# Kernel tuning notes

Measured on AMD Instinct MI355X. Metric: run time of the kernel, lower is better.

The kernel has to match this reference:

```python
import jax, jax.numpy as jnp
import numpy as np

N_P = 2048   # personality nodes
N_W = 89     # word nodes (fixed by user_word_adj[:, :89])
N_ALL = N_P + N_W
B = 16384    # users
E2 = 768     # sentence embedding size
UW = 313     # 89 word cols + 224 extra cols -> 32 + 224 = 256 for share1


def setup_inputs() -> dict:
    key = jax.random.key(0)
    ks = jax.random.split(key, 20)
    rn = lambda k, s, sc=0.1: (jax.random.normal(k, s, jnp.float32) * sc)
    pern_adj = jax.random.randint(ks[2], (N_P, N_P), 0, 2, jnp.int32)
    pern_adj = pern_adj.at[jnp.arange(N_P), jnp.arange(N_P)].set(1)
    word_pern_adj = jax.random.randint(ks[3], (N_ALL, N_ALL), 0, 2, jnp.int32)
    word_pern_adj = word_pern_adj.at[jnp.arange(N_ALL), jnp.arange(N_ALL)].set(1)
    return dict(
        pern_feature=rn(ks[0], (N_P, 256), 1.0),
        word_feature=rn(ks[1], (N_W, 256), 1.0),
        pern_adj=pern_adj,
        word_pern_adj=word_pern_adj,
        user_word_adj=jax.random.uniform(ks[4], (B, UW), jnp.float32),
        sentence_embed=rn(ks[5], (B, E2), 1.0),
        w1=rn(ks[6], (8, 256, 32)), a_src1=rn(ks[7], (8, 32)), a_dst1=rn(ks[8], (8, 32)), bias1=jnp.zeros((32,), jnp.float32),
        w2=rn(ks[9], (8, 256, 32)), a_src2=rn(ks[10], (8, 32)), a_dst2=rn(ks[11], (8, 32)), bias2=jnp.zeros((32,), jnp.float32),
        W_s1=rn(ks[12], (256, 128)), b_s1=jnp.zeros((128,), jnp.float32),
        W_s2=rn(ks[13], (E2, 128)), b_s2=jnp.zeros((128,), jnp.float32),
        W_f1=rn(ks[14], (128, 64)), b_f1=jnp.zeros((64,), jnp.float32),
        W_fa=rn(ks[15], (256, 128)), b_fa=jnp.zeros((128,), jnp.float32),
        W_fb=rn(ks[16], (128, 5)), b_fb=jnp.zeros((5,), jnp.float32),
    )


def gat(h, adj, w, a_src, a_dst, bias):
    # h: (n, f_in); w: (H, f_in, f_out); a_src/a_dst: (H, f_out); adj: (n, n) 0/1
    hp = jnp.einsum('nf,hfo->hno', h, w)                      # (H, n, f_out)
    e_src = jnp.einsum('hno,ho->hn', hp, a_src)               # (H, n)
    e_dst = jnp.einsum('hno,ho->hn', hp, a_dst)               # (H, n)
    e = jax.nn.leaky_relu(e_src[:, :, None] + e_dst[:, None, :], 0.2)  # (H, n, n)
    e = jnp.where(adj[None, :, :] > 0, e, jnp.float32(-1e9))
    attn = jax.nn.softmax(e, axis=-1)
    out = jnp.einsum('hnm,hmo->hno', attn, hp) + bias         # (H, n, f_out)
    return out, attn


def reference(pern_feature, word_feature, pern_adj, word_pern_adj,
              user_word_adj, sentence_embed,
              w1, a_src1, a_dst1, bias1, w2, a_src2, a_dst2, bias2,
              W_s1, b_s1, W_s2, b_s2, W_f1, b_f1, W_fa, b_fa, W_fb, b_fb):
    n_p = pern_feature.shape[0]
    # GAT 1 on personality graph
    h1, attn_pp = gat(pern_feature, pern_adj, w1, a_src1, a_dst1, bias1)
    h1 = jax.nn.elu(jnp.transpose(h1, (1, 0, 2)).reshape(n_p, -1))   # (n_p, 256)
    # dropout is identity at eval time
    h1_wp = jnp.concatenate([word_feature, h1], axis=0)               # (n_w+n_p, 256)
    # GAT 2 on word-personality graph, mean over heads
    h2, attn_wp = gat(h1_wp, word_pern_adj, w2, a_src2, a_dst2, bias2)
    h2 = h2.mean(axis=0)                                              # (n_w+n_p, 32)
    h2_word = h2[:word_feature.shape[0], :]                           # (89, 32)
    # user aggregation over word adjacency + row normalization
    x = user_word_adj[:, :N_W] @ h2_word                              # (B, 32)
    x_c = jnp.concatenate([x, user_word_adj[:, N_W:]], axis=1)        # (B, 256)
    x = x_c / x_c.sum(axis=1, keepdims=True)
    # dual heads
    output1 = x @ W_s1 + b_s1
    output2 = sentence_embed @ W_s2 + b_s2
    output1_new = output1 @ W_f1 + b_f1
    output2_new = output2 @ W_f1 + b_f1
    x_temp = jnp.concatenate([output1, output2], axis=1)
    x_temp = jax.nn.relu(x_temp @ W_fa + b_fa) @ W_fb + b_fb
    return (output1_new, output2_new, x_temp, attn_pp, attn_wp, x)
```

## Files before the change

kernel.cpp:

```cpp
#include <hip/hip_runtime.h>
#include <cstdint>
#include <cstddef>

#define N_P 2048
#define N_W 89
#define N_ALLC 2137
#define BQ 16384
#define E2C 768

typedef __attribute__((ext_vector_type(8))) short short8;
typedef __attribute__((ext_vector_type(4))) float float4v;

__device__ __forceinline__ float waveMax(float v){
#pragma unroll
  for (int o = 32; o > 0; o >>= 1) v = fmaxf(v, __shfl_down(v, o, 64));
  return v;
}
__device__ __forceinline__ float waveSum(float v){
#pragma unroll
  for (int o = 32; o > 0; o >>= 1) v += __shfl_down(v, o, 64);
  return v;
}
__device__ __forceinline__ unsigned short f2bf(float f){
  union { float f; unsigned int u; } v; v.f = f;
  unsigned int u = v.u;
  unsigned int r = (u + 0x7FFFu + ((u >> 16) & 1u)) >> 16;
  return (unsigned short)r;
}
__device__ __forceinline__ short8 cvt8(const float* p){
  float4 f0 = *(const float4*)p;
  float4 f1 = *(const float4*)(p + 4);
  short8 a;
  a[0] = (short)f2bf(f0.x); a[1] = (short)f2bf(f0.y);
  a[2] = (short)f2bf(f0.z); a[3] = (short)f2bf(f0.w);
  a[4] = (short)f2bf(f1.x); a[5] = (short)f2bf(f1.y);
  a[6] = (short)f2bf(f1.z); a[7] = (short)f2bf(f1.w);
  return a;
}

__device__ __forceinline__ void wpk_one(const float* __restrict__ W,
                                        unsigned short* __restrict__ out,
                                        int K, int N, int idx){
  if (idx >= K * N) return;
  int k = idx / N, n = idx - k * N;
  out[((size_t)((k >> 5) * 4 + ((k >> 3) & 3)) * N + n) * 8 + (k & 7)] = f2bf(W[idx]);
}

__global__ __launch_bounds__(256) void repack_all(
    const float* __restrict__ w1, float* __restrict__ wrm1,
    const float* __restrict__ w2, float* __restrict__ wrm2,
    const float* __restrict__ Ws1, unsigned short* __restrict__ ws1pk,
    const float* __restrict__ Ws2, unsigned short* __restrict__ ws2pk,
    const float* __restrict__ Wf1, unsigned short* __restrict__ wf1pk,
    const float* __restrict__ Wfa, unsigned short* __restrict__ wfapk,
    const float* __restrict__ wf, float* __restrict__ h1wp,
    const int* __restrict__ adj1, unsigned long long* __restrict__ bm1,
    const int* __restrict__ adj2, unsigned long long* __restrict__ bm2)
{
  int b = blockIdx.x, t = threadIdx.x;
  if (b < 256) {
    int idx = b * 256 + t;
    int f = idx >> 8, c = idx & 255;
    int h = c >> 5, o = c & 31;
    wrm1[idx] = w1[h * 8192 + f * 32 + o];
  } else if (b < 512) {
    int idx = (b - 256) * 256 + t;
    int f = idx >> 8, c = idx & 255;
    int h = c >> 5, o = c & 31;
    wrm2[idx] = w2[h * 8192 + f * 32 + o];
  } else if (b < 640) {
    wpk_one(Ws1, ws1pk, 256, 128, (b - 512) * 256 + t);
  } else if (b < 1024) {
    wpk_one(Ws2, ws2pk, 768, 128, (b - 640) * 256 + t);
  } else if (b < 1056) {
    wpk_one(Wf1, wf1pk, 128, 64, (b - 1024) * 256 + t);
  } else if (b < 1184) {
    wpk_one(Wfa, wfapk, 256, 128, (b - 1056) * 256 + t);
  } else if (b < 1273) {
    int idx = (b - 1184) * 256 + t;
    if (idx < N_W * 256) h1wp[idx] = wf[idx];
  } else if (b < 1529) {
    int r0 = (b - 1273) * 8;
    int wv = t >> 6, ln = t & 63;
    for (int rr = 0; rr < 8; ++rr) {
      int r = r0 + rr;
      const int* arow = adj1 + (size_t)r * N_P;
      for (int m0 = wv * 64; m0 < N_P; m0 += 256) {
        unsigned long long mask = __ballot(arow[m0 + ln] > 0);
        if (ln == 0) bm1[(size_t)r * 32 + (m0 >> 6)] = mask;
      }
    }
  } else {
    int r0 = (b - 1529) * 8;
    int wv = t >> 6, ln = t & 63;
    for (int rr = 0; rr < 8; ++rr) {
      int r = r0 + rr;
      if (r >= N_ALLC) break;
      const int* arow = adj2 + (size_t)r * N_ALLC;
      for (int m0 = wv * 64; m0 < 2176; m0 += 256) {
        int m = m0 + ln;
        unsigned long long mask = __ballot((m < N_ALLC) && (arow[m] > 0));
        if (ln == 0) bm2[(size_t)r * 34 + (m0 >> 6)] = mask;
      }
    }
  }
}

__global__ __launch_bounds__(256) void gemm_f32(
    const float* __restrict__ A, int lda,
    const float* __restrict__ B, int ldb,
    float* __restrict__ C, int ldc,
    int M, int N, int K)
{
  __shared__ __align__(16) float As[16][68];
  __shared__ __align__(16) float Bs[16][68];
  int t = threadIdx.x;
  int m0 = blockIdx.x * 64, n0 = blockIdx.y * 64;
  int tm = t >> 4, tn = t & 15;
  int ar = t >> 2, ak = (t & 3) * 4;
  int bk = t >> 4, bn = (t & 15) * 4;
  float acc[4][4] = {};
  for (int k0 = 0; k0 < K; k0 += 16) {
    float4 av = {0.f, 0.f, 0.f, 0.f};
    int arow = m0 + ar;
    if (arow < M) av = *(const float4*)(A + (size_t)arow * lda + k0 + ak);
    As[ak][ar] = av.x; As[ak + 1][ar] = av.y; As[ak + 2][ar] = av.z; As[ak + 3][ar] = av.w;
    *(float4*)&Bs[bk][bn] = *(const float4*)(B + (size_t)(k0 + bk) * ldb + n0 + bn);
    __syncthreads();
#pragma unroll
    for (int kk = 0; kk < 16; ++kk) {
      float4 a4 = *(const float4*)&As[kk][tm * 4];
      float4 b4 = *(const float4*)&Bs[kk][tn * 4];
      float a[4] = {a4.x, a4.y, a4.z, a4.w};
      float b[4] = {b4.x, b4.y, b4.z, b4.w};
#pragma unroll
      for (int i = 0; i < 4; ++i)
#pragma unroll
        for (int j = 0; j < 4; ++j) acc[i][j] += a[i] * b[j];
    }
    __syncthreads();
  }
#pragma unroll
  for (int i = 0; i < 4; ++i) {
    int row = m0 + tm * 4 + i;
    if (row < M) {
      float4 v;
      v.x = acc[i][0]; v.y = acc[i][1]; v.z = acc[i][2]; v.w = acc[i][3];
      *(float4*)(C + (size_t)row * ldc + n0 + tn * 4) = v;
    }
  }
}

__global__ __launch_bounds__(256) void esrc_edst(
    const float* __restrict__ hp,
    const float* __restrict__ a_src,
    const float* __restrict__ a_dst,
    float* __restrict__ es, float* __restrict__ ed,
    unsigned short* __restrict__ hppk,
    float* __restrict__ h2w, const float* __restrict__ b2,
    int N, int do_pack)
{
  __shared__ float sa[256], sd[256];
  int t = threadIdx.x;
  sa[t] = a_src[t]; sd[t] = a_dst[t];
  __syncthreads();
  int idx = blockIdx.x * 256 + t;
  if (h2w != nullptr && idx < N_W * 32) h2w[idx] = b2[idx & 31];
  if (idx >= N * 8) return;
  int n = idx >> 3, h = idx & 7;
  const float* hpp = hp + (size_t)n * 256 + h * 32;
  const float* ap = sa + h * 32;
  const float* dp = sd + h * 32;
  float s = 0.f, d = 0.f;
  float hv[32];
#pragma unroll
  for (int o = 0; o < 32; ++o) { hv[o] = hpp[o]; s += hv[o] * ap[o]; d += hv[o] * dp[o]; }
  es[h * N + n] = s; ed[h * N + n] = d;
  if (do_pack) {
    unsigned short* dst = hppk + (size_t)h * (N_P * 32)
                        + (size_t)((n >> 5) * 4 + ((n >> 3) & 3)) * 256 + (n & 7);
#pragma unroll
    for (int o = 0; o < 32; ++o) dst[o * 8] = f2bf(hv[o]);
  }
}

__global__ __launch_bounds__(256) void attn_softmax(
    const float* __restrict__ es, const float* __restrict__ ed,
    const unsigned long long* __restrict__ bm, int bstride,
    float* __restrict__ attn,
    int N)
{
  int h = blockIdx.x, n = blockIdx.y;
  int t = threadIdx.x, lane = t & 63, wid = t >> 6;
  __shared__ float red[4];
  float esv = es[h * N + n];
  const float* edh = ed + (size_t)h * N;
  const unsigned long long* brow = bm + (size_t)n * bstride;
  float v[9];
  float lmax = -3e38f;
#pragma unroll
  for (int i = 0; i < 9; ++i) {
    int m = i * 256 + t;
    float x = -3e38f;
    if (m < N) {
      float e = esv + edh[m];
      e = (e >= 0.f) ? e : 0.2f * e;
      x = ((brow[m >> 6] >> (m & 63)) & 1ULL) ? e : -1e9f;
    }
    v[i] = x; lmax = fmaxf(lmax, x);
  }
  lmax = waveMax(lmax);
  if (lane == 0) red[wid] = lmax;
  __syncthreads();
  float gmax = fmaxf(fmaxf(red[0], red[1]), fmaxf(red[2], red[3]));
  __syncthreads();
  float lsum = 0.f;
#pragma unroll
  for (int i = 0; i < 9; ++i) {
    int m = i * 256 + t;
    if (m < N) { float p = __expf(v[i] - gmax); v[i] = p; lsum += p; }
  }
  lsum = waveSum(lsum);
  if (lane == 0) red[wid] = lsum;
  __syncthreads();
  float inv = 1.f / (red[0] + red[1] + red[2] + red[3]);
  float* out = attn + ((size_t)h * N + n) * N;
#pragma unroll
  for (int i = 0; i < 9; ++i) {
    int m = i * 256 + t;
    if (m < N) out[m] = v[i] * inv;
  }
}

__global__ __launch_bounds__(256) void pv1_mfma(
    const float* __restrict__ attn,
    const unsigned short* __restrict__ hppk,
    const float* __restrict__ bias,
    float* __restrict__ h1wp)
{
  __shared__ float red[2][16][33];
  int t = threadIdx.x, w = t >> 6, lane = t & 63;
  int col = lane & 15, quad = lane >> 4;
  int kh = w >> 1, rh = (w & 1) * 16;
  int h = blockIdx.y;
  int row0 = blockIdx.x * 32;
  int rowA = row0 + rh + col;
  const float* arow = attn + ((size_t)h * N_P + rowA) * N_P + kh * 1024;
  const unsigned short* wb0 = hppk + (size_t)h * (N_P * 32) + (size_t)kh * 32768;
  float4v acc0 = {0.f, 0.f, 0.f, 0.f}, acc1 = {0.f, 0.f, 0.f, 0.f};
#pragma unroll 4
  for (int kk = 0; kk < 1024; kk += 32) {
    short8 a = cvt8(arow + kk + quad * 8);
    const unsigned short* wb = wb0 + ((size_t)((kk >> 5) * 4 + quad) * 32 + col) * 8;
    short8 b0 = *(const short8*)(wb);
    short8 b1 = *(const short8*)(wb + 128);
    acc0 = __builtin_amdgcn_mfma_f32_16x16x32_bf16(a, b0, acc0, 0, 0, 0);
    acc1 = __builtin_amdgcn_mfma_f32_16x16x32_bf16(a, b1, acc1, 0, 0, 0);
  }
  if (kh == 1) {
#pragma unroll
    for (int r = 0; r < 4; ++r) {
      red[w & 1][quad * 4 + r][col] = acc0[r];
      red[w & 1][quad * 4 + r][16 + col] = acc1[r];
    }
  }
  __syncthreads();
  if (kh == 0) {
    int rbase = row0 + rh + quad * 4;
#pragma unroll
    for (int r = 0; r < 4; ++r) {
      float v0 = acc0[r] + red[w & 1][quad * 4 + r][col] + bias[col];
      float v1 = acc1[r] + red[w & 1][quad * 4 + r][16 + col] + bias[16 + col];
      v0 = (v0 > 0.f) ? v0 : expm1f(v0);
      v1 = (v1 > 0.f) ? v1 : expm1f(v1);
      float* dst = h1wp + (size_t)(N_W + rbase + r) * 256 + h * 32;
      dst[col] = v0; dst[16 + col] = v1;
    }
  }
}

__global__ __launch_bounds__(256) void pv2(
    const float* __restrict__ attn,
    const float* __restrict__ hp,
    float* __restrict__ h2w)
{
  int n = blockIdx.x, h = blockIdx.y;
  int t = threadIdx.x, g = t >> 5, o = t & 31;
  const float* arow = attn + ((size_t)h * N_ALLC + n) * N_ALLC;
  float acc = 0.f;
  for (int m = g; m < N_ALLC; m += 8) acc += arow[m] * hp[(size_t)m * 256 + h * 32 + o];
  __shared__ float pv[8][33];
  pv[g][o] = acc;
  __syncthreads();
  if (t < 32) {
    float s = 0.f;
#pragma unroll
    for (int gg = 0; gg < 8; ++gg) s += pv[gg][t];
    atomicAdd(&h2w[n * 32 + t], s * 0.125f);
  }
}

__global__ __launch_bounds__(256) void xnorm_kernel(
    const float* __restrict__ uwa,
    const float* __restrict__ h2w,
    float* __restrict__ xout)
{
  __shared__ float urow[4][320];
  __shared__ float sh2w[N_W * 32];
  __shared__ float px[4][2][32];
  __shared__ float xh[4][33];
  __shared__ float inv[4];
  int t = threadIdx.x;
  int b0 = blockIdx.x * 4;
  for (int i = t; i < N_W * 32; i += 256) sh2w[i] = h2w[i];
  for (int idx = t; idx < 4 * 313; idx += 256) {
    int r = idx / 313, j = idx - r * 313;
    urow[r][j] = uwa[(size_t)(b0 + r) * 313 + j];
  }
  __syncthreads();
  {
    int r = t >> 6, q = (t >> 5) & 1, o = t & 31;
    float s = 0.f;
    int i0 = q * 45, i1 = q ? N_W : 45;
    for (int i = i0; i < i1; ++i) s += urow[r][i] * sh2w[i * 32 + o];
    px[r][q][o] = s;
  }
  __syncthreads();
  if (t < 128) {
    int r = t >> 5, o = t & 31;
    xh[r][o] = px[r][0][o] + px[r][1][o];
  }
  __syncthreads();
  int lane = t & 63, w = t >> 6;
  float ls = 0.f;
  for (int c = lane; c < 256; c += 64) {
    float v = (c < 32) ? xh[w][c] : urow[w][89 + c - 32];
    ls += v;
  }
  ls = waveSum(ls);
  if (lane == 0) inv[w] = 1.f / ls;
  __syncthreads();
  for (int idx = t; idx < 1024; idx += 256) {
    int r = idx >> 8, c = idx & 255;
    float v = (c < 32) ? xh[r][c] : urow[r][89 + c - 32];
    xout[(size_t)(b0 + r) * 256 + c] = v * inv[r];
  }
}

__global__ __launch_bounds__(256) void o12_fused(
    const float* __restrict__ x,
    const float* __restrict__ sent,
    const unsigned short* __restrict__ ws1pk,
    const unsigned short* __restrict__ ws2pk,
    const float* __restrict__ bs1,
    const float* __restrict__ bs2,
    unsigned short* __restrict__ o12bf)
{
  int t = threadIdx.x, w = t >> 6, lane = t & 63;
  int col = lane & 15, quad = lane >> 4;
  int rowA = blockIdx.x * 64 + w * 16 + col;
  int half = blockIdx.y;
  const float* A = half ? (sent + (size_t)rowA * E2C) : (x + (size_t)rowA * 256);
  const unsigned short* wpk = half ? ws2pk : ws1pk;
  const float* bias = half ? bs2 : bs1;
  int K = half ? E2C : 256;
  float4v acc[8];
#pragma unroll
  for (int i = 0; i < 8; ++i) acc[i] = (float4v){0.f, 0.f, 0.f, 0.f};
#pragma unroll 4
  for (int k0 = 0; k0 < K; k0 += 32) {
    short8 a = cvt8(A + k0 + quad * 8);
    const unsigned short* wb = wpk + ((size_t)((k0 >> 5) * 4 + quad) * 128 + col) * 8;
#pragma unroll
    for (int nt = 0; nt < 8; ++nt)
      acc[nt] = __builtin_amdgcn_mfma_f32_16x16x32_bf16(a, *(const short8*)(wb + nt * 128), acc[nt], 0, 0, 0);
  }
  int rbase = blockIdx.x * 64 + w * 16 + quad * 4;
  int cb = half * 128;
#pragma unroll
  for (int nt = 0; nt < 8; ++nt) {
    int c = nt * 16 + col;
    float bv = bias[c];
#pragma unroll
    for (int r = 0; r < 4; ++r)
      o12bf[(size_t)(rbase + r) * 256 + cb + c] = f2bf(acc[nt][r] + bv);
  }
}

__global__ __launch_bounds__(256) void tail_fused(
    const unsigned short* __restrict__ o12bf,
    const unsigned short* __restrict__ wf1pk,
    const unsigned short* __restrict__ wfapk,
    const float* __restrict__ bf1,
    const float* __restrict__ bfa,
    const float* __restrict__ Wfb,
    const float* __restrict__ bfb,
    float* __restrict__ o1n, float* __restrict__ o2n, float* __restrict__ xt)
{
  __shared__ float sWfb[640];
  int t = threadIdx.x;
  for (int i = t; i < 640; i += 256) sWfb[i] = Wfb[i];
  __syncthreads();
  int w = t >> 6, lane = t & 63;
  int col = lane & 15, quad = lane >> 4;
  int rowA = blockIdx.x * 64 + w * 16 + col;
  const unsigned short* ar = o12bf + (size_t)rowA * 256;
  float4v aT[8], a1[4], a2[4];
#pragma unroll
  for (int i = 0; i < 8; ++i) aT[i] = (float4v){0.f, 0.f, 0.f, 0.f};
#pragma unroll
  for (int i = 0; i < 4; ++i) { a1[i] = (float4v){0.f, 0.f, 0.f, 0.f}; a2[i] = (float4v){0.f, 0.f, 0.f, 0.f}; }
#pragma unroll
  for (int k0 = 0; k0 < 128; k0 += 32) {
    short8 a = *(const short8*)(ar + k0 + quad * 8);
    const unsigned short* wbT = wfapk + ((size_t)((k0 >> 5) * 4 + quad) * 128 + col) * 8;
    const unsigned short* wb1 = wf1pk + ((size_t)((k0 >> 5) * 4 + quad) * 64 + col) * 8;
#pragma unroll
    for (int nt = 0; nt < 8; ++nt)
      aT[nt] = __builtin_amdgcn_mfma_f32_16x16x32_bf16(a, *(const short8*)(wbT + nt * 128), aT[nt], 0, 0, 0);
#pragma unroll
    for (int nt = 0; nt < 4; ++nt)
      a1[nt] = __builtin_amdgcn_mfma_f32_16x16x32_bf16(a, *(const short8*)(wb1 + nt * 128), a1[nt], 0, 0, 0);
  }
#pragma unroll
  for (int k0 = 128; k0 < 256; k0 += 32) {
    short8 a = *(const short8*)(ar + k0 + quad * 8);
    const unsigned short* wbT = wfapk + ((size_t)((k0 >> 5) * 4 + quad) * 128 + col) * 8;
    const unsigned short* wb1 = wf1pk + ((size_t)(((k0 - 128) >> 5) * 4 + quad) * 64 + col) * 8;
#pragma unroll
    for (int nt = 0; nt < 8; ++nt)
      aT[nt] = __builtin_amdgcn_mfma_f32_16x16x32_bf16(a, *(const short8*)(wbT + nt * 128), aT[nt], 0, 0, 0);
#pragma unroll
    for (int nt = 0; nt < 4; ++nt)
      a2[nt] = __builtin_amdgcn_mfma_f32_16x16x32_bf16(a, *(const short8*)(wb1 + nt * 128), a2[nt], 0, 0, 0);
  }
  int rbase = blockIdx.x * 64 + w * 16 + quad * 4;
#pragma unroll
  for (int nt = 0; nt < 4; ++nt) {
    int c = nt * 16 + col;
    float b1v = bf1[c];
#pragma unroll
    for (int r = 0; r < 4; ++r) {
      o1n[(size_t)(rbase + r) * 64 + c] = a1[nt][r] + b1v;
      o2n[(size_t)(rbase + r) * 64 + c] = a2[nt][r] + b1v;
    }
  }
  float xp[4][5] = {};
#pragma unroll
  for (int nt = 0; nt < 8; ++nt) {
    int c = nt * 16 + col;
    float bav = bfa[c];
#pragma unroll
    for (int r = 0; r < 4; ++r) {
      float tv = fmaxf(aT[nt][r] + bav, 0.f);
#pragma unroll
      for (int q = 0; q < 5; ++q) xp[r][q] += tv * sWfb[c * 5 + q];
    }
  }
#pragma unroll
  for (int m = 1; m <= 8; m <<= 1) {
#pragma unroll
    for (int r = 0; r < 4; ++r)
#pragma unroll
      for (int q = 0; q < 5; ++q) xp[r][q] += __shfl_xor(xp[r][q], m, 64);
  }
  if (col == 0) {
#pragma unroll
    for (int r = 0; r < 4; ++r)
#pragma unroll
      for (int q = 0; q < 5; ++q) xt[(size_t)(rbase + r) * 5 + q] = xp[r][q] + bfb[q];
  }
}

extern "C" void kernel_launch(void* const* d_in, const int* in_sizes, int n_in,
                              void* d_out, int out_size, void* d_ws, size_t ws_size,
                              hipStream_t stream)
{
  const float* pf   = (const float*)d_in[0];
  const float* wf   = (const float*)d_in[1];
  const int*   adj1 = (const int*)d_in[2];
  const int*   adj2 = (const int*)d_in[3];
  const float* uwa  = (const float*)d_in[4];
  const float* sent = (const float*)d_in[5];
  const float* w1   = (const float*)d_in[6];
  const float* as1  = (const float*)d_in[7];
  const float* ad1  = (const float*)d_in[8];
  const float* b1   = (const float*)d_in[9];
  const float* w2   = (const float*)d_in[10];
  const float* as2  = (const float*)d_in[11];
  const float* ad2  = (const float*)d_in[12];
  const float* b2   = (const float*)d_in[13];
  const float* Ws1  = (const float*)d_in[14];
  const float* bs1  = (const float*)d_in[15];
  const float* Ws2  = (const float*)d_in[16];
  const float* bs2  = (const float*)d_in[17];
  const float* Wf1  = (const float*)d_in[18];
  const float* bf1  = (const float*)d_in[19];
  const float* Wfa  = (const float*)d_in[20];
  const float* bfa  = (const float*)d_in[21];
  const float* Wfb  = (const float*)d_in[22];
  const float* bfb  = (const float*)d_in[23];

  float* ws = (float*)d_ws;
  float* wrm1 = ws;
  float* wrm2 = wrm1 + 65536;
  float* hp1  = wrm2 + 65536;
  float* hp2  = hp1 + (size_t)N_P * 256;
  float* es1v = hp2 + (size_t)N_ALLC * 256;
  float* ed1v = es1v + 8 * N_P;
  float* es2v = ed1v + 8 * N_P;
  float* ed2v = es2v + 17152;
  float* h1wp = ed2v + 17152;
  float* h2w  = h1wp + (size_t)N_ALLC * 256;
  unsigned long long* bm1 = (unsigned long long*)(h2w + 2880);
  unsigned long long* bm2 = bm1 + (size_t)2048 * 32;
  unsigned short* o12bf = (unsigned short*)(bm2 + 72704);
  unsigned short* hp1pk = o12bf + (size_t)BQ * 256;
  unsigned short* ws1pk = hp1pk + 8 * N_P * 32;
  unsigned short* ws2pk = ws1pk + 256 * 128;
  unsigned short* wf1pk = ws2pk + 768 * 128;
  unsigned short* wfapk = wf1pk + 128 * 64;

  float* out = (float*)d_out;
  float* out_o1n = out;
  float* out_o2n = out + (size_t)BQ * 64;
  float* out_xt  = out + (size_t)BQ * 128;
  float* out_app = out_xt + (size_t)BQ * 5;
  float* out_awp = out_app + (size_t)8 * N_P * N_P;
  float* out_x   = out_awp + (size_t)8 * N_ALLC * N_ALLC;

  repack_all<<<1797, 256, 0, stream>>>(w1, wrm1, w2, wrm2, Ws1, ws1pk, Ws2, ws2pk,
                                       Wf1, wf1pk, Wfa, wfapk, wf, h1wp,
                                       adj1, bm1, adj2, bm2);
  gemm_f32<<<dim3(32, 4), 256, 0, stream>>>(pf, 256, wrm1, 256, hp1, 256, N_P, 256, 256);
  esrc_edst<<<(N_P * 8 + 255) / 256, 256, 0, stream>>>(hp1, as1, ad1, es1v, ed1v,
                                                       hp1pk, nullptr, nullptr, N_P, 1);
  attn_softmax<<<dim3(8, N_P), 256, 0, stream>>>(es1v, ed1v, bm1, 32, out_app, N_P);
  pv1_mfma<<<dim3(64, 8), 256, 0, stream>>>(out_app, hp1pk, b1, h1wp);
  gemm_f32<<<dim3(34, 4), 256, 0, stream>>>(h1wp, 256, wrm2, 256, hp2, 256, N_ALLC, 256, 256);
  esrc_edst<<<(N_ALLC * 8 + 255) / 256, 256, 0, stream>>>(hp2, as2, ad2, es2v, ed2v,
                                                          nullptr, h2w, b2, N_ALLC, 0);
  attn_softmax<<<dim3(8, N_ALLC), 256, 0, stream>>>(es2v, ed2v, bm2, 34, out_awp, N_ALLC);
  pv2<<<dim3(N_W, 8), 256, 0, stream>>>(out_awp, hp2, h2w);
  xnorm_kernel<<<BQ / 4, 256, 0, stream>>>(uwa, h2w, out_x);
  o12_fused<<<dim3(BQ / 64, 2), 256, 0, stream>>>(out_x, sent, ws1pk, ws2pk, bs1, bs2, o12bf);
  tail_fused<<<BQ / 64, 256, 0, stream>>>(o12bf, wf1pk, wfapk, bf1, bfa, Wfb, bfb,
                                          out_o1n, out_o2n, out_xt);
}
```

Before: 682.2 us.

## Fuse GAT1 softmax into the attention-times-values MFMA kernel

Replaces the separate attn_softmax and pv1_mfma launches for the first GAT layer with one kernel. It recomputes the masked leaky-relu logits from the per-node scores and the bitmask, takes the row max and sum in two passes, then writes the normalized attention and feeds it straight into the bf16 MFMA. This drops the re-read of the 8x2048x2048 fp32 attention matrix, at the cost of computing the logits three times. The grid is only 512 blocks, so the softmax work now runs at lower parallelism than the old per-row launch.

Measured after the change: 696.0 us. 1.02x slower.

```diff
diff --git a/kernel.cpp b/kernel.cpp
--- a/kernel.cpp
+++ b/kernel.cpp
@@ -232,25 +232,98 @@
   }
 }
 
-__global__ __launch_bounds__(256) void pv1_mfma(
-    const float* __restrict__ attn,
+__global__ __launch_bounds__(256) void sm_pv1(
+    const float* __restrict__ es, const float* __restrict__ ed,
+    const unsigned long long* __restrict__ bm,
     const unsigned short* __restrict__ hppk,
     const float* __restrict__ bias,
+    float* __restrict__ attn,
     float* __restrict__ h1wp)
 {
+  __shared__ float pmax[2][32];
+  __shared__ float psum[2][32];
+  __shared__ float sM[32], sInv[32];
   __shared__ float red[2][16][33];
   int t = threadIdx.x, w = t >> 6, lane = t & 63;
   int col = lane & 15, quad = lane >> 4;
-  int kh = w >> 1, rh = (w & 1) * 16;
+  int kh = w >> 1, rhs = w & 1;
   int h = blockIdx.y;
   int row0 = blockIdx.x * 32;
-  int rowA = row0 + rh + col;
-  const float* arow = attn + ((size_t)h * N_P + rowA) * N_P + kh * 1024;
+  const float* edh = ed + (size_t)h * N_P + kh * 1024;
+
+  for (int r = 0; r < 16; ++r) {
+    int n = row0 + rhs * 16 + r;
+    float esv = es[h * N_P + n];
+    const unsigned long long* brow = bm + (size_t)n * 32 + kh * 16;
+    float lmax = -3e38f;
+#pragma unroll 4
+    for (int s = 0; s < 16; ++s) {
+      unsigned long long mk = brow[s];
+      float e = esv + edh[s * 64 + lane];
+      e = (e >= 0.f) ? e : 0.2f * e;
+      float x = ((mk >> lane) & 1ULL) ? e : -1e9f;
+      lmax = fmaxf(lmax, x);
+    }
+    lmax = waveMax(lmax);
+    if (lane == 0) pmax[kh][rhs * 16 + r] = lmax;
+  }
+  __syncthreads();
+  if (t < 32) sM[t] = fmaxf(pmax[0][t], pmax[1][t]);
+  __syncthreads();
+
+  for (int r = 0; r < 16; ++r) {
+    int n = row0 + rhs * 16 + r;
+    float esv = es[h * N_P + n];
+    float M = sM[rhs * 16 + r];
+    const unsigned long long* brow = bm + (size_t)n * 32 + kh * 16;
+    float lsum = 0.f;
+#pragma unroll 4
+    for (int s = 0; s < 16; ++s) {
+      unsigned long long mk = brow[s];
+      float e = esv + edh[s * 64 + lane];
+      e = (e >= 0.f) ? e : 0.2f * e;
+      float x = ((mk >> lane) & 1ULL) ? e : -1e9f;
+      lsum += __expf(x - M);
+    }
+    lsum = waveSum(lsum);
+    if (lane == 0) psum[kh][rhs * 16 + r] = lsum;
+  }
+  __syncthreads();
+  if (t < 32) sInv[t] = 1.f / (psum[0][t] + psum[1][t]);
+  __syncthreads();
+
+  int nrow = row0 + rhs * 16 + col;
+  float esv = es[h * N_P + nrow];
+  float M = sM[rhs * 16 + col];
+  float inv = sInv[rhs * 16 + col];
+  const unsigned long long* brow = bm + (size_t)nrow * 32;
+  float* arow = attn + ((size_t)h * N_P + nrow) * N_P + kh * 1024;
+  const float* edq = edh + quad * 8;
   const unsigned short* wb0 = hppk + (size_t)h * (N_P * 32) + (size_t)kh * 32768;
   float4v acc0 = {0.f, 0.f, 0.f, 0.f}, acc1 = {0.f, 0.f, 0.f, 0.f};
 #pragma unroll 4
   for (int kk = 0; kk < 1024; kk += 32) {
-    short8 a = cvt8(arow + kk + quad * 8);
+    int kc = kk + quad * 8;
+    unsigned long long mw = brow[(kh * 1024 + kc) >> 6];
+    int sh = (kk & 63) + quad * 8;
+    float4 e0 = *(const float4*)(edq + kk);
+    float4 e1 = *(const float4*)(edq + kk + 4);
+    float ev[8] = {e0.x, e0.y, e0.z, e0.w, e1.x, e1.y, e1.z, e1.w};
+    float p[8];
+#pragma unroll
+    for (int j = 0; j < 8; ++j) {
+      float e = esv + ev[j];
+      e = (e >= 0.f) ? e : 0.2f * e;
+      float x = ((mw >> (sh + j)) & 1ULL) ? e : -1e9f;
+      p[j] = __expf(x - M) * inv;
+    }
+    float4 o0 = {p[0], p[1], p[2], p[3]};
+    float4 o1 = {p[4], p[5], p[6], p[7]};
+    *(float4*)(arow + kc) = o0;
+    *(float4*)(arow + kc + 4) = o1;
+    short8 a;
+#pragma unroll
+    for (int j = 0; j < 8; ++j) a[j] = (short)f2bf(p[j]);
     const unsigned short* wb = wb0 + ((size_t)((kk >> 5) * 4 + quad) * 32 + col) * 8;
     short8 b0 = *(const short8*)(wb);
     short8 b1 = *(const short8*)(wb + 128);
@@ -260,17 +333,17 @@
   if (kh == 1) {
 #pragma unroll
     for (int r = 0; r < 4; ++r) {
-      red[w & 1][quad * 4 + r][col] = acc0[r];
-      red[w & 1][quad * 4 + r][16 + col] = acc1[r];
+      red[rhs][quad * 4 + r][col] = acc0[r];
+      red[rhs][quad * 4 + r][16 + col] = acc1[r];
     }
   }
   __syncthreads();
   if (kh == 0) {
-    int rbase = row0 + rh + quad * 4;
+    int rbase = row0 + rhs * 16 + quad * 4;
 #pragma unroll
     for (int r = 0; r < 4; ++r) {
-      float v0 = acc0[r] + red[w & 1][quad * 4 + r][col] + bias[col];
-      float v1 = acc1[r] + red[w & 1][quad * 4 + r][16 + col] + bias[16 + col];
+      float v0 = acc0[r] + red[rhs][quad * 4 + r][col] + bias[col];
+      float v1 = acc1[r] + red[rhs][quad * 4 + r][16 + col] + bias[16 + col];
       v0 = (v0 > 0.f) ? v0 : expm1f(v0);
       v1 = (v1 > 0.f) ? v1 : expm1f(v1);
       float* dst = h1wp + (size_t)(N_W + rbase + r) * 256 + h * 32;
@@ -535,8 +608,7 @@
   gemm_f32<<<dim3(32, 4), 256, 0, stream>>>(pf, 256, wrm1, 256, hp1, 256, N_P, 256, 256);
   esrc_edst<<<(N_P * 8 + 255) / 256, 256, 0, stream>>>(hp1, as1, ad1, es1v, ed1v,
                                                        hp1pk, nullptr, nullptr, N_P, 1);
-  attn_softmax<<<dim3(8, N_P), 256, 0, stream>>>(es1v, ed1v, bm1, 32, out_app, N_P);
-  pv1_mfma<<<dim3(64, 8), 256, 0, stream>>>(out_app, hp1pk, b1, h1wp);
+  sm_pv1<<<dim3(64, 8), 256, 0, stream>>>(es1v, ed1v, bm1, hp1pk, b1, out_app, h1wp);
   gemm_f32<<<dim3(34, 4), 256, 0, stream>>>(h1wp, 256, wrm2, 256, hp2, 256, N_ALLC, 256, 256);
   esrc_edst<<<(N_ALLC * 8 + 255) / 256, 256, 0, stream>>>(hp2, as2, ad2, es2v, ed2v,
                                                           nullptr, h2w, b2, N_ALLC, 0);
```
